# Kernel optimization log

Hardware: AMD Instinct MI355X
Metric: run time of the kernel (lower is better)

Reference implementation:

```python
import jax, jax.numpy as jnp
import numpy as np

B, N, D, H, DFF = 4096, 64, 256, 8, 1024
HD = D // H

def _ln(x, g, b):
    m = jnp.mean(x, axis=-1, keepdims=True)
    v = jnp.var(x, axis=-1, keepdims=True)
    return (x - m) / jnp.sqrt(v + 1e-5) * g + b


def setup_inputs() -> dict:
    key = jax.random.key(0)
    ks = jax.random.split(key, 16)
    s = jnp.float32(0.02)
    def rn(k, shape):
        return jax.random.normal(k, shape, dtype=jnp.float32) * s
    d2 = D // 2
    return {
        "x": jax.random.normal(ks[0], (B, N, 1), dtype=jnp.float32),
        "ve_w1": rn(ks[1], (1, d2)), "ve_b1": jnp.zeros((d2,), jnp.float32),
        "ve_w2": rn(ks[2], (d2, D)), "ve_b2": jnp.zeros((D,), jnp.float32),
        "pos_emb": rn(ks[3], (100, D)),
        "attn_in_w": rn(ks[4], (D, 3 * D)), "attn_in_b": jnp.zeros((3 * D,), jnp.float32),
        "attn_out_w": rn(ks[5], (D, D)), "attn_out_b": jnp.zeros((D,), jnp.float32),
        "ffn_w1": rn(ks[6], (D, DFF)), "ffn_b1": jnp.zeros((DFF,), jnp.float32),
        "ffn_w2": rn(ks[7], (DFF, D)), "ffn_b2": jnp.zeros((D,), jnp.float32),
        "ln1_g": jnp.ones((D,), jnp.float32), "ln1_b": jnp.zeros((D,), jnp.float32),
        "ln2_g": jnp.ones((D,), jnp.float32), "ln2_b": jnp.zeros((D,), jnp.float32),
        "rank_emb": rn(ks[8], (100, D)),
        "q_w": rn(ks[9], (D, D)), "q_b": jnp.zeros((D,), jnp.float32),
        "k_w": rn(ks[10], (D, D)), "k_b": jnp.zeros((D,), jnp.float32),
    }


def reference(x, ve_w1, ve_b1, ve_w2, ve_b2, pos_emb, attn_in_w, attn_in_b,
              attn_out_w, attn_out_b, ffn_w1, ffn_b1, ffn_w2, ffn_b2,
              ln1_g, ln1_b, ln2_g, ln2_b, rank_emb, q_w, q_b, k_w, k_b):
    # ---- encode ----
    v = jax.nn.relu(x @ ve_w1 + ve_b1) @ ve_w2 + ve_b2          # [B,N,D]
    h = v + pos_emb[:N][None]                                    # broadcast pos embed
    qkv = h @ attn_in_w + attn_in_b
    q, k, vv = jnp.split(qkv, 3, axis=-1)
    split_heads = lambda t: t.reshape(B, N, H, HD).transpose(0, 2, 1, 3)
    q, k, vv = split_heads(q), split_heads(k), split_heads(vv)
    scores = jnp.einsum('bhqd,bhkd->bhqk', q, k) / jnp.sqrt(jnp.float32(HD))
    attn = jax.nn.softmax(scores, axis=-1)
    ao = jnp.einsum('bhqk,bhkd->bhqd', attn, vv).transpose(0, 2, 1, 3).reshape(B, N, D)
    ao = ao @ attn_out_w + attn_out_b
    h = _ln(h + ao, ln1_g, ln1_b)
    ff = jax.nn.relu(h @ ffn_w1 + ffn_b1) @ ffn_w2 + ffn_b2
    enc = _ln(h + ff, ln2_g, ln2_b)                              # [B,N,D]

    # ---- pointer decode (greedy, coverage mask) ----
    Q = rank_emb[:N] @ q_w + q_b                                 # [N,D] rank queries
    K = enc @ k_w + k_b                                          # [B,N,D]
    base = jnp.einsum('td,bnd->tbn', Q, K)                       # [N,B,N] unmasked logits per rank
    bidx = jnp.arange(B)

    def step(mask, base_t):
        logits_t = jnp.where(mask > 0, base_t, -jnp.inf)         # masked_fill
        chosen = jnp.argmax(logits_t, axis=-1)                   # greedy pick
        mask = mask.at[bidx, chosen].set(0.0)                    # scatter mask update
        return mask, logits_t

    mask0 = jnp.ones((B, N), jnp.float32)
    _, all_logits = jax.lax.scan(step, mask0, base)              # [N,B,N]
    return all_logits.transpose(1, 0, 2)                         # [B,N,N]
```

## Files before the change

### kernel.cpp

```cpp
#include <hip/hip_runtime.h>
#include <math.h>


typedef __attribute__((ext_vector_type(8))) short bf16x8;
typedef __attribute__((ext_vector_type(4))) float f32x4;

#define NEG_FILL (-3.0e38f)

#define U_Q    0
#define U_VE   2048
#define U_QKV  6144
#define U_WO   30720
#define U_F1   38912
#define U_F2   71680
#define U_KW   104448
#define U_TOT  112640

#define SH_H  0
#define SH_A  16384
#define SH_SHORTS 32768
#define FB_FLOATS 4096
#define LDS_BYTES (SH_SHORTS*2 + FB_FLOATS*4)

__device__ __forceinline__ unsigned short f2bf(float f){
  unsigned u = __float_as_uint(f);
  return (unsigned short)((u + 0x7FFFu + ((u>>16)&1u)) >> 16);
}
__device__ __forceinline__ float bf2f(unsigned short h){
  return __uint_as_float(((unsigned)h) << 16);
}

#define MFMA(a,b,c) __builtin_amdgcn_mfma_f32_16x16x32_bf16((a),(b),(c),0,0,0)
#define SM_SCALE 0.17677669529663687f

__global__ void __launch_bounds__(256) prep_q(const float* __restrict__ rank_emb,
                                              const float* __restrict__ q_w,
                                              const float* __restrict__ q_b,
                                              short* __restrict__ wsp) {
    int t = blockIdx.x;
    int c = threadIdx.x;
    float acc = q_b[c];
    for (int d = 0; d < 256; d += 4) {
        acc += rank_emb[t*256 + d + 0] * q_w[(d+0)*256 + c]
             + rank_emb[t*256 + d + 1] * q_w[(d+1)*256 + c]
             + rank_emb[t*256 + d + 2] * q_w[(d+2)*256 + c]
             + rank_emb[t*256 + d + 3] * q_w[(d+3)*256 + c];
    }
    int kb = c >> 5, lane = ((c>>3)&3)*16 + (t&15), j = c & 7;
    int u = ((t>>4)*8 + kb)*64 + lane;
    wsp[(U_Q + u)*8 + j] = (short)f2bf(acc);
}

__global__ void __launch_bounds__(256) prep_w(const float* __restrict__ ve_w2,
                                              const float* __restrict__ attn_in_w,
                                              const float* __restrict__ attn_out_w,
                                              const float* __restrict__ ffn_w1,
                                              const float* __restrict__ ffn_w2,
                                              const float* __restrict__ k_w,
                                              short* __restrict__ wsp) {
    int r = blockIdx.x*256 + threadIdx.x;
    const float* w; int N, K, base;
    if (r < 4096)                { w = ve_w2;      N = 256;  K = 128;  base = U_VE;  }
    else if ((r -= 4096)  < 24576) { w = attn_in_w;  N = 768;  K = 256;  base = U_QKV; }
    else if ((r -= 24576) < 8192)  { w = attn_out_w; N = 256;  K = 256;  base = U_WO;  }
    else if ((r -= 8192)  < 32768) { w = ffn_w1;     N = 1024; K = 256;  base = U_F1;  }
    else if ((r -= 32768) < 32768) { w = ffn_w2;     N = 256;  K = 1024; base = U_F2;  }
    else     { r -= 32768;           w = k_w;        N = 256;  K = 256;  base = U_KW;  }
    int KB = K >> 5;
    int lane = r & 63;
    int kb   = (r >> 6) % KB;
    int nt   = r / (64 * KB);
    int n  = nt*16 + (lane & 15);
    int k0 = kb*32 + (lane >> 4)*8;
    bf16x8 hv;
#pragma unroll
    for (int j = 0; j < 8; j++) hv[j] = (short)f2bf(w[(size_t)(k0 + j)*N + n]);
    *(bf16x8*)&wsp[(size_t)(base + r) * 8] = hv;
}

__global__ void __launch_bounds__(512, 4) fused_kernel(
    const float* __restrict__ x,
    const float* __restrict__ ve_w1, const float* __restrict__ ve_b1,
    const float* __restrict__ ve_b2,
    const float* __restrict__ pos_emb,
    const float* __restrict__ attn_in_b,
    const float* __restrict__ attn_out_b,
    const float* __restrict__ ffn_b1, const float* __restrict__ ffn_b2,
    const float* __restrict__ ln1_g, const float* __restrict__ ln1_b,
    const float* __restrict__ ln2_g, const float* __restrict__ ln2_b,
    const float* __restrict__ k_b,
    const short* __restrict__ wsp,
    float* __restrict__ out)
{
    extern __shared__ short sm[];
    float* smf  = (float*)(sm + SH_SHORTS);
    float* SB   = smf;

    const int tid  = threadIdx.x;
    const int b    = blockIdx.x;
    const int w    = tid >> 6;
    const int lane = tid & 63;
    const int quad = lane >> 4;
    const int lcol = lane & 15;

    const bf16x8* wsv = (const bf16x8*)wsp;
    const bf16x8* HFu = (const bf16x8*)&sm[SH_H];
    bf16x8* HFw = (bf16x8*)&sm[SH_H];

#pragma unroll
    for (int i = 0; i < 2; i++) {
        int u = tid + i*512;
        int l3 = u & 63, kb = (u >> 6) & 3, mt = u >> 8;
        int m  = mt*16 + (l3 & 15);
        int k0 = kb*32 + (l3 >> 4)*8;
        float xv = x[b*64 + m];
        bf16x8 hv;
#pragma unroll
        for (int j = 0; j < 8; j++) {
            float f = xv * ve_w1[k0 + j] + ve_b1[k0 + j];
            hv[j] = (short)f2bf(f > 0.f ? f : 0.f);
        }
        *(bf16x8*)&sm[SH_A + u*8] = hv;
    }
    __syncthreads();

    {
        f32x4 acc[2][4];
#pragma unroll
        for (int s = 0; s < 2; s++)
#pragma unroll
            for (int mi = 0; mi < 4; mi++) acc[s][mi] = (f32x4){0.f,0.f,0.f,0.f};
#pragma unroll
        for (int kb = 0; kb < 4; kb++) {
            bf16x8 bh0 = wsv[U_VE + ((w    )*4+kb)*64 + lane];
            bf16x8 bh1 = wsv[U_VE + ((w + 8)*4+kb)*64 + lane];
#pragma unroll
            for (int mi = 0; mi < 4; mi++) {
                bf16x8 ah = *(const bf16x8*)&sm[SH_A + ((mi*4+kb)*64 + lane)*8];
                acc[0][mi] = MFMA(ah, bh0, acc[0][mi]);
                acc[1][mi] = MFMA(ah, bh1, acc[1][mi]);
            }
        }
        __syncthreads();
#pragma unroll
        for (int s = 0; s < 2; s++) {
            int n = (w + s*8)*16 + lcol;
#pragma unroll
            for (int mi = 0; mi < 4; mi++)
#pragma unroll
                for (int reg = 0; reg < 4; reg++) {
                    int m = mi*16 + quad*4 + reg;
                    float val = acc[s][mi][reg] + ve_b2[n] + pos_emb[m*256 + n];
                    int kb2 = n >> 5, l2 = ((n>>3)&3)*16 + (m&15), j2 = n & 7;
                    sm[SH_H + ((mi*8 + kb2)*64 + l2)*8 + j2] = (short)f2bf(val);
                }
        }
    }
    __syncthreads();

    f32x4 aoacc[2][4];
#pragma unroll
    for (int s = 0; s < 2; s++)
#pragma unroll
        for (int mi = 0; mi < 4; mi++) aoacc[s][mi] = (f32x4){0.f,0.f,0.f,0.f};

    const int il = w & 3;
    const int eo = il >> 1, ch = il & 1;

    auto qkv_phase = [&](int p) {
        int ntv = 32 + 4*p + il;
        if (w < 4) {
            int ntg = 4*p + il;
            f32x4 acc[4];
#pragma unroll
            for (int mi = 0; mi < 4; mi++) acc[mi] = (f32x4){0.f,0.f,0.f,0.f};
#pragma unroll
            for (int kb = 0; kb < 8; kb++) {
                bf16x8 bh = wsv[U_QKV + (ntg*8+kb)*64 + lane];
#pragma unroll
                for (int mi = 0; mi < 4; mi++)
                    acc[mi] = MFMA(HFu[(mi*8+kb)*64 + lane], bh, acc[mi]);
            }
#pragma unroll
            for (int mi = 0; mi < 4; mi++)
#pragma unroll
                for (int reg = 0; reg < 4; reg++) {
                    int m  = mi*16 + quad*4 + reg;
                    int cc = ch*16 + lcol;
                    short hv = (short)f2bf(acc[mi][reg] + attn_in_b[ntg*16 + lcol]);
                    int l2 = ((cc>>3)&3)*16 + (m&15), j2 = cc & 7;
                    sm[SH_A + eo*2048 + (mi*64 + l2)*8 + j2] = hv;
                }
            f32x4 va[2];
            va[0] = (f32x4){0.f,0.f,0.f,0.f}; va[1] = (f32x4){0.f,0.f,0.f,0.f};
#pragma unroll
            for (int kb = 0; kb < 8; kb++) {
                bf16x8 bh = wsv[U_QKV + (ntv*8+kb)*64 + lane];
                va[0] = MFMA(HFu[(0*8+kb)*64 + lane], bh, va[0]);
                va[1] = MFMA(HFu[(1*8+kb)*64 + lane], bh, va[1]);
            }
#pragma unroll
            for (int mi = 0; mi < 2; mi++)
#pragma unroll
                for (int reg = 0; reg < 4; reg++) {
                    int m  = mi*16 + quad*4 + reg;
                    int cc = ch*16 + lcol;
                    short hv = (short)f2bf(va[mi][reg] + attn_in_b[ntv*16 + lcol]);
                    int kb2 = m >> 5;
                    int l2 = ((m>>3)&3)*16 + lcol, j2 = m & 7;
                    sm[SH_A + 8192 + eo*2048 + ((ch*2 + kb2)*64 + l2)*8 + j2] = hv;
                }
        } else {
            int ntg = 16 + 4*p + il;
            f32x4 acc[4];
#pragma unroll
            for (int mi = 0; mi < 4; mi++) acc[mi] = (f32x4){0.f,0.f,0.f,0.f};
#pragma unroll
            for (int kb = 0; kb < 8; kb++) {
                bf16x8 bh = wsv[U_QKV + (ntg*8+kb)*64 + lane];
#pragma unroll
                for (int mi = 0; mi < 4; mi++)
                    acc[mi] = MFMA(HFu[(mi*8+kb)*64 + lane], bh, acc[mi]);
            }
#pragma unroll
            for (int mi = 0; mi < 4; mi++)
#pragma unroll
                for (int reg = 0; reg < 4; reg++) {
                    int m  = mi*16 + quad*4 + reg;
                    int cc = ch*16 + lcol;
                    short hv = (short)f2bf(acc[mi][reg] + attn_in_b[ntg*16 + lcol]);
                    int l2 = ((cc>>3)&3)*16 + (m&15), j2 = cc & 7;
                    sm[SH_A + 4096 + eo*2048 + ((m>>4)*64 + l2)*8 + j2] = hv;
                }
            f32x4 va[2];
            va[0] = (f32x4){0.f,0.f,0.f,0.f}; va[1] = (f32x4){0.f,0.f,0.f,0.f};
#pragma unroll
            for (int kb = 0; kb < 8; kb++) {
                bf16x8 bh = wsv[U_QKV + (ntv*8+kb)*64 + lane];
                va[0] = MFMA(HFu[(2*8+kb)*64 + lane], bh, va[0]);
                va[1] = MFMA(HFu[(3*8+kb)*64 + lane], bh, va[1]);
            }
#pragma unroll
            for (int mi2 = 0; mi2 < 2; mi2++)
#pragma unroll
                for (int reg = 0; reg < 4; reg++) {
                    int m  = (mi2+2)*16 + quad*4 + reg;
                    int cc = ch*16 + lcol;
                    short hv = (short)f2bf(va[mi2][reg] + attn_in_b[ntv*16 + lcol]);
                    int kb2 = m >> 5;
                    int l2 = ((m>>3)&3)*16 + lcol, j2 = m & 7;
                    sm[SH_A + 8192 + eo*2048 + ((ch*2 + kb2)*64 + l2)*8 + j2] = hv;
                }
        }
    };

    auto scores_sm = [&](int e) {
        if (w < 4) {
            int mi = w;
            bf16x8 ah = *(const bf16x8*)&sm[SH_A + e*2048 + (mi*64 + lane)*8];
            f32x4 sa[4];
#pragma unroll
            for (int ni = 0; ni < 4; ni++) {
                bf16x8 bh = *(const bf16x8*)&sm[SH_A + 4096 + e*2048 + (ni*64 + lane)*8];
                f32x4 z = (f32x4){0.f,0.f,0.f,0.f};
                sa[ni] = MFMA(ah, bh, z);
            }
#pragma unroll
            for (int reg = 0; reg < 4; reg++) {
                float v0 = sa[0][reg]*SM_SCALE, v1 = sa[1][reg]*SM_SCALE;
                float v2 = sa[2][reg]*SM_SCALE, v3 = sa[3][reg]*SM_SCALE;
                float mx = fmaxf(fmaxf(v0,v1), fmaxf(v2,v3));
#pragma unroll
                for (int off = 8; off >= 1; off >>= 1) mx = fmaxf(mx, __shfl_xor(mx, off, 64));
                v0 = __expf(v0-mx); v1 = __expf(v1-mx); v2 = __expf(v2-mx); v3 = __expf(v3-mx);
                float s = v0+v1+v2+v3;
#pragma unroll
                for (int off = 8; off >= 1; off >>= 1) s += __shfl_xor(s, off, 64);
                float inv = 1.0f / s;
                float pr[4] = {v0*inv, v1*inv, v2*inv, v3*inv};
                int mr = quad*4 + reg;
#pragma unroll
                for (int ni = 0; ni < 4; ni++) {
                    int u  = mi*2 + (ni>>1);
                    int l2 = ((ni*2 + (lcol>>3))&3)*16 + mr;
                    sm[SH_SHORTS + e*4096 + u*512 + l2*8 + (lcol&7)] = (short)f2bf(pr[ni]);
                }
            }
        }
    };

    auto pv_phase = [&](int e) {
        int mi = w & 3, ni = w >> 2;
        f32x4 pv = (f32x4){0.f,0.f,0.f,0.f};
#pragma unroll
        for (int kb = 0; kb < 2; kb++) {
            bf16x8 ah = *(const bf16x8*)&sm[SH_SHORTS + e*4096 + ((mi*2+kb)*64 + lane)*8];
            bf16x8 bh = *(const bf16x8*)&sm[SH_A + 8192 + e*2048 + ((ni*2+kb)*64 + lane)*8];
            pv = MFMA(ah, bh, pv);
        }
#pragma unroll
        for (int reg = 0; reg < 4; reg++) {
            int m = mi*16 + quad*4 + reg;
            int c = ni*16 + lcol;
            int l2 = ((c>>3)&3)*16 + (m&15), j2 = c & 7;
            sm[SH_A + 12288 + e*2048 + (mi*64 + l2)*8 + j2] = (short)f2bf(pv[reg]);
        }
    };

    auto wo_phase = [&](int hh, int e) {
        bf16x8 bh0 = wsv[U_WO + ((w    )*8 + hh)*64 + lane];
        bf16x8 bh1 = wsv[U_WO + ((w + 8)*8 + hh)*64 + lane];
#pragma unroll
        for (int mi = 0; mi < 4; mi++) {
            bf16x8 ah = *(const bf16x8*)&sm[SH_A + 12288 + e*2048 + (mi*64 + lane)*8];
            aoacc[0][mi] = MFMA(ah, bh0, aoacc[0][mi]);
            aoacc[1][mi] = MFMA(ah, bh1, aoacc[1][mi]);
        }
    };

    qkv_phase(0);
    __syncthreads();
    for (int p = 0; p < 4; p++) {
        scores_sm(0);
        __syncthreads();
        pv_phase(0);  scores_sm(1);
        __syncthreads();
        wo_phase(2*p, 0);  pv_phase(1);
        __syncthreads();
        wo_phase(2*p+1, 1);
        if (p < 3) qkv_phase(p+1);
        __syncthreads();
    }

#pragma unroll
    for (int s = 0; s < 2; s++) {
        int n = (w + s*8)*16 + lcol;
#pragma unroll
        for (int mi = 0; mi < 4; mi++)
#pragma unroll
            for (int reg = 0; reg < 4; reg++) {
                int m  = mi*16 + quad*4 + reg;
                int kb2 = n >> 5, l2 = ((n>>3)&3)*16 + (m&15), j2 = n & 7;
                int uu = ((mi*8 + kb2)*64 + l2)*8 + j2;
                float val = bf2f((unsigned short)sm[SH_H + uu]) + aoacc[s][mi][reg] + attn_out_b[n];
                sm[SH_H + uu] = (short)f2bf(val);
            }
    }
    __syncthreads();

    auto layernormFO = [&](const float* __restrict__ g, const float* __restrict__ bt) {
        int m = tid >> 3, kb = tid & 7;
        int ub = ((m>>4)*8 + kb)*64 + (m&15);
        bf16x8 h0 = HFu[ub +  0];
        bf16x8 h1 = HFu[ub + 16];
        bf16x8 h2 = HFu[ub + 32];
        bf16x8 h3 = HFu[ub + 48];
        float v[32];
#pragma unroll
        for (int j = 0; j < 8; j++) {
            v[j]    = bf2f((unsigned short)h0[j]);
            v[8+j]  = bf2f((unsigned short)h1[j]);
            v[16+j] = bf2f((unsigned short)h2[j]);
            v[24+j] = bf2f((unsigned short)h3[j]);
        }
        float sum = 0.f;
#pragma unroll
        for (int i = 0; i < 32; i++) sum += v[i];
#pragma unroll
        for (int off = 4; off >= 1; off >>= 1) sum += __shfl_xor(sum, off, 64);
        float mean = sum * (1.0f/256.0f);
        float s2 = 0.f;
#pragma unroll
        for (int i = 0; i < 32; i++) { float d = v[i] - mean; s2 += d*d; }
#pragma unroll
        for (int off = 4; off >= 1; off >>= 1) s2 += __shfl_xor(s2, off, 64);
        float r = 1.0f / sqrtf(s2 * (1.0f/256.0f) + 1e-5f);
#pragma unroll
        for (int q = 0; q < 4; q++) {
            bf16x8 oh;
#pragma unroll
            for (int j = 0; j < 8; j++) {
                int k = kb*32 + q*8 + j;
                oh[j] = (short)f2bf((v[q*8+j] - mean) * r * g[k] + bt[k]);
            }
            HFw[ub + q*16] = oh;
        }
        __syncthreads();
    };
    layernormFO(ln1_g, ln1_b);

    f32x4 f2acc[2][4];
#pragma unroll
    for (int s = 0; s < 2; s++)
#pragma unroll
        for (int mi = 0; mi < 4; mi++) f2acc[s][mi] = (f32x4){0.f,0.f,0.f,0.f};

    for (int c = 0; c < 4; c++) {
        f32x4 a1[4];
#pragma unroll
        for (int mi = 0; mi < 4; mi++) a1[mi] = (f32x4){0.f,0.f,0.f,0.f};
#pragma unroll
        for (int kb = 0; kb < 8; kb++) {
            bf16x8 bh = wsv[U_F1 + ((c*16 + w)*8 + kb)*64 + lane];
#pragma unroll
            for (int mi = 0; mi < 4; mi++) {
                bf16x8 ah = HFu[(mi*8+kb)*64 + lane];
                a1[mi] = MFMA(ah, bh, a1[mi]);
            }
        }
        __syncthreads();
#pragma unroll
        for (int mi = 0; mi < 4; mi++)
#pragma unroll
            for (int reg = 0; reg < 4; reg++) {
                int m = mi*16 + quad*4 + reg;
                int n = (c*16 + w)*16 + lcol;
                float val = a1[mi][reg] + ffn_b1[n];
                val = val > 0.f ? val : 0.f;
                int kk = w*16 + lcol;
                int kb2 = kk >> 5, l2 = ((kk>>3)&3)*16 + (m&15), j2 = kk & 7;
                sm[SH_A + ((mi*8 + kb2)*64 + l2)*8 + j2] = (short)f2bf(val);
            }
#pragma unroll
        for (int mi = 0; mi < 4; mi++) a1[mi] = (f32x4){0.f,0.f,0.f,0.f};
#pragma unroll
        for (int kb = 0; kb < 8; kb++) {
            bf16x8 bh = wsv[U_F1 + ((c*16 + w + 8)*8 + kb)*64 + lane];
#pragma unroll
            for (int mi = 0; mi < 4; mi++) {
                bf16x8 ah = HFu[(mi*8+kb)*64 + lane];
                a1[mi] = MFMA(ah, bh, a1[mi]);
            }
        }
#pragma unroll
        for (int mi = 0; mi < 4; mi++)
#pragma unroll
            for (int reg = 0; reg < 4; reg++) {
                int m = mi*16 + quad*4 + reg;
                int n = (c*16 + w + 8)*16 + lcol;
                float val = a1[mi][reg] + ffn_b1[n];
                val = val > 0.f ? val : 0.f;
                int kk = (w + 8)*16 + lcol;
                int kb2 = kk >> 5, l2 = ((kk>>3)&3)*16 + (m&15), j2 = kk & 7;
                sm[SH_A + ((mi*8 + kb2)*64 + l2)*8 + j2] = (short)f2bf(val);
            }
        __syncthreads();
#pragma unroll 2
        for (int kbl = 0; kbl < 8; kbl++) {
            bf16x8 bh0 = wsv[U_F2 + ((w    )*32 + c*8 + kbl)*64 + lane];
            bf16x8 bh1 = wsv[U_F2 + ((w + 8)*32 + c*8 + kbl)*64 + lane];
#pragma unroll
            for (int mi = 0; mi < 4; mi++) {
                bf16x8 ah = *(const bf16x8*)&sm[SH_A + ((mi*8+kbl)*64 + lane)*8];
                f2acc[0][mi] = MFMA(ah, bh0, f2acc[0][mi]);
                f2acc[1][mi] = MFMA(ah, bh1, f2acc[1][mi]);
            }
        }
    }
    __syncthreads();
#pragma unroll
    for (int s = 0; s < 2; s++) {
        int n = (w + s*8)*16 + lcol;
#pragma unroll
        for (int mi = 0; mi < 4; mi++)
#pragma unroll
            for (int reg = 0; reg < 4; reg++) {
                int m  = mi*16 + quad*4 + reg;
                int kb2 = n >> 5, l2 = ((n>>3)&3)*16 + (m&15), j2 = n & 7;
                int uu = ((mi*8 + kb2)*64 + l2)*8 + j2;
                float val = bf2f((unsigned short)sm[SH_H + uu]) + f2acc[s][mi][reg] + ffn_b2[n];
                sm[SH_H + uu] = (short)f2bf(val);
            }
    }
    __syncthreads();
    layernormFO(ln2_g, ln2_b);

    {
        f32x4 kacc[2][4];
#pragma unroll
        for (int s = 0; s < 2; s++)
#pragma unroll
            for (int mi = 0; mi < 4; mi++) kacc[s][mi] = (f32x4){0.f,0.f,0.f,0.f};
#pragma unroll
        for (int kb = 0; kb < 8; kb++) {
            bf16x8 bh0 = wsv[U_KW + ((w    )*8+kb)*64 + lane];
            bf16x8 bh1 = wsv[U_KW + ((w + 8)*8+kb)*64 + lane];
#pragma unroll
            for (int mi = 0; mi < 4; mi++) {
                bf16x8 ah = HFu[(mi*8+kb)*64 + lane];
                kacc[0][mi] = MFMA(ah, bh0, kacc[0][mi]);
                kacc[1][mi] = MFMA(ah, bh1, kacc[1][mi]);
            }
        }
        __syncthreads();
#pragma unroll
        for (int s = 0; s < 2; s++) {
            int n = (w + s*8)*16 + lcol;
#pragma unroll
            for (int mi = 0; mi < 4; mi++)
#pragma unroll
                for (int reg = 0; reg < 4; reg++) {
                    int m = mi*16 + quad*4 + reg;
                    int nt2 = m >> 4, kb2 = n >> 5;
                    int l2 = ((n>>3)&3)*16 + (m&15), j2 = n & 7;
                    sm[SH_H + ((nt2*8 + kb2)*64 + l2)*8 + j2] =
                        (short)f2bf(kacc[s][mi][reg] + k_b[n]);
                }
        }
    }
    __syncthreads();

#pragma unroll
    for (int it = 0; it < 2; it++) {
        int t = w*2 + it;
        int mi = t >> 2, nt = t & 3;
        f32x4 sacc = (f32x4){0.f,0.f,0.f,0.f};
#pragma unroll
        for (int kb = 0; kb < 8; kb++) {
            bf16x8 bh = HFu[(nt*8+kb)*64 + lane];
            bf16x8 ah = wsv[U_Q + (mi*8+kb)*64 + lane];
            sacc = MFMA(ah, bh, sacc);
        }
#pragma unroll
        for (int reg = 0; reg < 4; reg++) {
            int tt = mi*16 + quad*4 + reg;
            int n = nt*16 + lcol;
            SB[tt*64 + (n ^ ((tt&7)<<2))] = sacc[reg];
        }
    }
    __syncthreads();

    if (tid < 64) {
        int ln = tid;
        bool alive = true;
        float* outb = out + (size_t)b * (64*64);
        for (int t = 0; t < 64; t++) {
            float v  = SB[t*64 + (ln ^ ((t&7)<<2))];
            float lv = alive ? v : NEG_FILL;
            outb[t*64 + ln] = lv;
            float bv = lv;
#pragma unroll
            for (int off = 32; off >= 1; off >>= 1)
                bv = fmaxf(bv, __shfl_xor(bv, off, 64));
            unsigned long long mk = __ballot(lv == bv);
            int bi = __ffsll(mk) - 1;
            if (bi == ln) alive = false;
        }
    }
}

extern "C" void kernel_launch(void* const* d_in, const int* in_sizes, int n_in,
                              void* d_out, int out_size, void* d_ws, size_t ws_size,
                              hipStream_t stream) {
    (void)in_sizes; (void)n_in; (void)out_size; (void)ws_size;
    const float* x          = (const float*)d_in[0];
    const float* ve_w1      = (const float*)d_in[1];
    const float* ve_b1      = (const float*)d_in[2];
    const float* ve_w2      = (const float*)d_in[3];
    const float* ve_b2      = (const float*)d_in[4];
    const float* pos_emb    = (const float*)d_in[5];
    const float* attn_in_w  = (const float*)d_in[6];
    const float* attn_in_b  = (const float*)d_in[7];
    const float* attn_out_w = (const float*)d_in[8];
    const float* attn_out_b = (const float*)d_in[9];
    const float* ffn_w1     = (const float*)d_in[10];
    const float* ffn_b1     = (const float*)d_in[11];
    const float* ffn_w2     = (const float*)d_in[12];
    const float* ffn_b2     = (const float*)d_in[13];
    const float* ln1_g      = (const float*)d_in[14];
    const float* ln1_b      = (const float*)d_in[15];
    const float* ln2_g      = (const float*)d_in[16];
    const float* ln2_b      = (const float*)d_in[17];
    const float* rank_emb   = (const float*)d_in[18];
    const float* q_w        = (const float*)d_in[19];
    const float* q_b        = (const float*)d_in[20];
    const float* k_w        = (const float*)d_in[21];
    const float* k_b        = (const float*)d_in[22];
    float* outp = (float*)d_out;
    short* wsp  = (short*)d_ws;

    (void)hipFuncSetAttribute((const void*)fused_kernel,
                              hipFuncAttributeMaxDynamicSharedMemorySize,
                              (int)LDS_BYTES);

    hipLaunchKernelGGL(prep_q, dim3(64), dim3(256), 0, stream, rank_emb, q_w, q_b, wsp);
    hipLaunchKernelGGL(prep_w, dim3(432), dim3(256), 0, stream,
                       ve_w2, attn_in_w, attn_out_w, ffn_w1, ffn_w2, k_w, wsp);
    hipLaunchKernelGGL(fused_kernel, dim3(4096), dim3(512), LDS_BYTES, stream,
                       x, ve_w1, ve_b1, ve_b2, pos_emb,
                       attn_in_b, attn_out_b,
                       ffn_b1, ffn_b2,
                       ln1_g, ln1_b, ln2_g, ln2_b,
                       k_b, (const short*)wsp, outp);
}
```

Baseline: 934.2 us.

## XOR-swizzle LDS fragment layout and pack bf16 pairs on conversion

Applies an XOR swizzle (lane ^ (lane>>4)) to every shared-memory bf16 fragment buffer, on both the scatter writes and the MFMA operand reads, so the strided scalar stores from accumulator tiles spread across LDS banks instead of colliding. The float-to-bf16 conversions are reorganized to convert pairs at once and hoist bias loads out of inner loops, and the V-transpose stores become 32-bit writes. The swizzle must match exactly across every producer and consumer of each buffer, which adds index arithmetic and risks correctness if any path is missed.

```diff
diff --git a/kernel.cpp b/kernel.cpp
--- a/kernel.cpp
+++ b/kernel.cpp
@@ -4,6 +4,7 @@
 
 typedef __attribute__((ext_vector_type(8))) short bf16x8;
 typedef __attribute__((ext_vector_type(4))) float f32x4;
+typedef __attribute__((ext_vector_type(4))) unsigned u32x4;
 
 #define NEG_FILL (-3.0e38f)
 
@@ -28,6 +29,9 @@
 }
 __device__ __forceinline__ float bf2f(unsigned short h){
   return __uint_as_float(((unsigned)h) << 16);
+}
+__device__ __forceinline__ unsigned pk2(float a, float b){
+  return (unsigned)f2bf(a) | ((unsigned)f2bf(b) << 16);
 }
 
 #define MFMA(a,b,c) __builtin_amdgcn_mfma_f32_16x16x32_bf16((a),(b),(c),0,0,0)
@@ -102,10 +106,10 @@
     const int lane = tid & 63;
     const int quad = lane >> 4;
     const int lcol = lane & 15;
+    const int slane = lane ^ (lane >> 4);
 
     const bf16x8* wsv = (const bf16x8*)wsp;
     const bf16x8* HFu = (const bf16x8*)&sm[SH_H];
-    bf16x8* HFw = (bf16x8*)&sm[SH_H];
 
 #pragma unroll
     for (int i = 0; i < 2; i++) {
@@ -114,13 +118,17 @@
         int m  = mt*16 + (l3 & 15);
         int k0 = kb*32 + (l3 >> 4)*8;
         float xv = x[b*64 + m];
-        bf16x8 hv;
+        float f[8];
 #pragma unroll
         for (int j = 0; j < 8; j++) {
-            float f = xv * ve_w1[k0 + j] + ve_b1[k0 + j];
-            hv[j] = (short)f2bf(f > 0.f ? f : 0.f);
-        }
-        *(bf16x8*)&sm[SH_A + u*8] = hv;
+            float t0 = xv * ve_w1[k0 + j] + ve_b1[k0 + j];
+            f[j] = t0 > 0.f ? t0 : 0.f;
+        }
+        u32x4 hv;
+        hv[0] = pk2(f[0], f[1]); hv[1] = pk2(f[2], f[3]);
+        hv[2] = pk2(f[4], f[5]); hv[3] = pk2(f[6], f[7]);
+        int sl3 = l3 ^ (l3 >> 4);
+        *(u32x4*)&sm[SH_A + ((u & ~63) | sl3)*8] = hv;
     }
     __syncthreads();
 
@@ -136,7 +144,7 @@
             bf16x8 bh1 = wsv[U_VE + ((w + 8)*4+kb)*64 + lane];
 #pragma unroll
             for (int mi = 0; mi < 4; mi++) {
-                bf16x8 ah = *(const bf16x8*)&sm[SH_A + ((mi*4+kb)*64 + lane)*8];
+                bf16x8 ah = *(const bf16x8*)&sm[SH_A + ((mi*4+kb)*64 + slane)*8];
                 acc[0][mi] = MFMA(ah, bh0, acc[0][mi]);
                 acc[1][mi] = MFMA(ah, bh1, acc[1][mi]);
             }
@@ -145,15 +153,24 @@
 #pragma unroll
         for (int s = 0; s < 2; s++) {
             int n = (w + s*8)*16 + lcol;
-#pragma unroll
-            for (int mi = 0; mi < 4; mi++)
+            int hi = (n>>3)&3, kb2 = n>>5, j2 = n&7;
+#pragma unroll
+            for (int mi = 0; mi < 4; mi++) {
+                float vv[4];
 #pragma unroll
                 for (int reg = 0; reg < 4; reg++) {
                     int m = mi*16 + quad*4 + reg;
-                    float val = acc[s][mi][reg] + ve_b2[n] + pos_emb[m*256 + n];
-                    int kb2 = n >> 5, l2 = ((n>>3)&3)*16 + (m&15), j2 = n & 7;
-                    sm[SH_H + ((mi*8 + kb2)*64 + l2)*8 + j2] = (short)f2bf(val);
-                }
+                    vv[reg] = acc[s][mi][reg] + ve_b2[n] + pos_emb[m*256 + n];
+                }
+#pragma unroll
+                for (int rp = 0; rp < 2; rp++) {
+                    unsigned r = pk2(vv[2*rp], vv[2*rp+1]);
+                    int m0 = quad*4 + 2*rp;
+                    int gbase = (mi*8 + kb2)*64 + hi*16;
+                    sm[SH_H + (gbase + ((m0  )^hi))*8 + j2] = (short)r;
+                    sm[SH_H + (gbase + ((m0+1)^hi))*8 + j2] = (short)(r >> 16);
+                }
+            }
         }
     }
     __syncthreads();
@@ -169,6 +186,8 @@
 
     auto qkv_phase = [&](int p) {
         int ntv = 32 + 4*p + il;
+        int cc = ch*16 + lcol;
+        int hic = (cc>>3)&3, j2c = cc&7;
         if (w < 4) {
             int ntg = 4*p + il;
             f32x4 acc[4];
@@ -179,36 +198,38 @@
                 bf16x8 bh = wsv[U_QKV + (ntg*8+kb)*64 + lane];
 #pragma unroll
                 for (int mi = 0; mi < 4; mi++)
-                    acc[mi] = MFMA(HFu[(mi*8+kb)*64 + lane], bh, acc[mi]);
-            }
+                    acc[mi] = MFMA(HFu[(mi*8+kb)*64 + slane], bh, acc[mi]);
+            }
+            float bq = attn_in_b[ntg*16 + lcol];
 #pragma unroll
             for (int mi = 0; mi < 4; mi++)
 #pragma unroll
-                for (int reg = 0; reg < 4; reg++) {
-                    int m  = mi*16 + quad*4 + reg;
-                    int cc = ch*16 + lcol;
-                    short hv = (short)f2bf(acc[mi][reg] + attn_in_b[ntg*16 + lcol]);
-                    int l2 = ((cc>>3)&3)*16 + (m&15), j2 = cc & 7;
-                    sm[SH_A + eo*2048 + (mi*64 + l2)*8 + j2] = hv;
+                for (int rp = 0; rp < 2; rp++) {
+                    unsigned r = pk2(acc[mi][2*rp] + bq, acc[mi][2*rp+1] + bq);
+                    int m0 = quad*4 + 2*rp;
+                    int gbase = SH_A + eo*2048 + (mi*64 + hic*16)*8;
+                    sm[gbase + (((m0  )^hic))*8 + j2c] = (short)r;
+                    sm[gbase + (((m0+1)^hic))*8 + j2c] = (short)(r >> 16);
                 }
             f32x4 va[2];
             va[0] = (f32x4){0.f,0.f,0.f,0.f}; va[1] = (f32x4){0.f,0.f,0.f,0.f};
 #pragma unroll
             for (int kb = 0; kb < 8; kb++) {
                 bf16x8 bh = wsv[U_QKV + (ntv*8+kb)*64 + lane];
-                va[0] = MFMA(HFu[(0*8+kb)*64 + lane], bh, va[0]);
-                va[1] = MFMA(HFu[(1*8+kb)*64 + lane], bh, va[1]);
-            }
+                va[0] = MFMA(HFu[(0*8+kb)*64 + slane], bh, va[0]);
+                va[1] = MFMA(HFu[(1*8+kb)*64 + slane], bh, va[1]);
+            }
+            float bv = attn_in_b[ntv*16 + lcol];
 #pragma unroll
             for (int mi = 0; mi < 2; mi++)
 #pragma unroll
-                for (int reg = 0; reg < 4; reg++) {
-                    int m  = mi*16 + quad*4 + reg;
-                    int cc = ch*16 + lcol;
-                    short hv = (short)f2bf(va[mi][reg] + attn_in_b[ntv*16 + lcol]);
-                    int kb2 = m >> 5;
-                    int l2 = ((m>>3)&3)*16 + lcol, j2 = m & 7;
-                    sm[SH_A + 8192 + eo*2048 + ((ch*2 + kb2)*64 + l2)*8 + j2] = hv;
+                for (int rp = 0; rp < 2; rp++) {
+                    unsigned r = pk2(va[mi][2*rp] + bv, va[mi][2*rp+1] + bv);
+                    int m0 = mi*16 + quad*4 + 2*rp;
+                    int kb2 = m0>>5, hi2 = (m0>>3)&3;
+                    int X = SH_A + 8192 + eo*2048
+                          + (((ch*2 + kb2)*64 + hi2*16 + (lcol^hi2)))*8 + (m0&7);
+                    *(unsigned*)&sm[X] = r;
                 }
         } else {
             int ntg = 16 + 4*p + il;
@@ -220,36 +241,38 @@
                 bf16x8 bh = wsv[U_QKV + (ntg*8+kb)*64 + lane];
 #pragma unroll
                 for (int mi = 0; mi < 4; mi++)
-                    acc[mi] = MFMA(HFu[(mi*8+kb)*64 + lane], bh, acc[mi]);
-            }
+                    acc[mi] = MFMA(HFu[(mi*8+kb)*64 + slane], bh, acc[mi]);
+            }
+            float bk = attn_in_b[ntg*16 + lcol];
 #pragma unroll
             for (int mi = 0; mi < 4; mi++)
 #pragma unroll
-                for (int reg = 0; reg < 4; reg++) {
-                    int m  = mi*16 + quad*4 + reg;
-                    int cc = ch*16 + lcol;
-                    short hv = (short)f2bf(acc[mi][reg] + attn_in_b[ntg*16 + lcol]);
-                    int l2 = ((cc>>3)&3)*16 + (m&15), j2 = cc & 7;
-                    sm[SH_A + 4096 + eo*2048 + ((m>>4)*64 + l2)*8 + j2] = hv;
+                for (int rp = 0; rp < 2; rp++) {
+                    unsigned r = pk2(acc[mi][2*rp] + bk, acc[mi][2*rp+1] + bk);
+                    int m0 = quad*4 + 2*rp;
+                    int gbase = SH_A + 4096 + eo*2048 + (mi*64 + hic*16)*8;
+                    sm[gbase + (((m0  )^hic))*8 + j2c] = (short)r;
+                    sm[gbase + (((m0+1)^hic))*8 + j2c] = (short)(r >> 16);
                 }
             f32x4 va[2];
             va[0] = (f32x4){0.f,0.f,0.f,0.f}; va[1] = (f32x4){0.f,0.f,0.f,0.f};
 #pragma unroll
             for (int kb = 0; kb < 8; kb++) {
                 bf16x8 bh = wsv[U_QKV + (ntv*8+kb)*64 + lane];
-                va[0] = MFMA(HFu[(2*8+kb)*64 + lane], bh, va[0]);
-                va[1] = MFMA(HFu[(3*8+kb)*64 + lane], bh, va[1]);
-            }
+                va[0] = MFMA(HFu[(2*8+kb)*64 + slane], bh, va[0]);
+                va[1] = MFMA(HFu[(3*8+kb)*64 + slane], bh, va[1]);
+            }
+            float bv = attn_in_b[ntv*16 + lcol];
 #pragma unroll
             for (int mi2 = 0; mi2 < 2; mi2++)
 #pragma unroll
-                for (int reg = 0; reg < 4; reg++) {
-                    int m  = (mi2+2)*16 + quad*4 + reg;
-                    int cc = ch*16 + lcol;
-                    short hv = (short)f2bf(va[mi2][reg] + attn_in_b[ntv*16 + lcol]);
-                    int kb2 = m >> 5;
-                    int l2 = ((m>>3)&3)*16 + lcol, j2 = m & 7;
-                    sm[SH_A + 8192 + eo*2048 + ((ch*2 + kb2)*64 + l2)*8 + j2] = hv;
+                for (int rp = 0; rp < 2; rp++) {
+                    unsigned r = pk2(va[mi2][2*rp] + bv, va[mi2][2*rp+1] + bv);
+                    int m0 = (mi2+2)*16 + quad*4 + 2*rp;
+                    int kb2 = m0>>5, hi2 = (m0>>3)&3;
+                    int X = SH_A + 8192 + eo*2048
+                          + (((ch*2 + kb2)*64 + hi2*16 + (lcol^hi2)))*8 + (m0&7);
+                    *(unsigned*)&sm[X] = r;
                 }
         }
     };
@@ -257,14 +280,17 @@
     auto scores_sm = [&](int e) {
         if (w < 4) {
             int mi = w;
-            bf16x8 ah = *(const bf16x8*)&sm[SH_A + e*2048 + (mi*64 + lane)*8];
+            bf16x8 ah = *(const bf16x8*)&sm[SH_A + e*2048 + (mi*64 + slane)*8];
             f32x4 sa[4];
 #pragma unroll
             for (int ni = 0; ni < 4; ni++) {
-                bf16x8 bh = *(const bf16x8*)&sm[SH_A + 4096 + e*2048 + (ni*64 + lane)*8];
+                bf16x8 bh = *(const bf16x8*)&sm[SH_A + 4096 + e*2048 + (ni*64 + slane)*8];
                 f32x4 z = (f32x4){0.f,0.f,0.f,0.f};
                 sa[ni] = MFMA(ah, bh, z);
             }
+            int lo3 = lcol>>3, j2 = lcol&7;
+            int hiA = lo3, hiB = 2 + lo3;
+            int pbase = SH_SHORTS + e*4096;
 #pragma unroll
             for (int reg = 0; reg < 4; reg++) {
                 float v0 = sa[0][reg]*SM_SCALE, v1 = sa[1][reg]*SM_SCALE;
@@ -277,14 +303,13 @@
 #pragma unroll
                 for (int off = 8; off >= 1; off >>= 1) s += __shfl_xor(s, off, 64);
                 float inv = 1.0f / s;
-                float pr[4] = {v0*inv, v1*inv, v2*inv, v3*inv};
                 int mr = quad*4 + reg;
-#pragma unroll
-                for (int ni = 0; ni < 4; ni++) {
-                    int u  = mi*2 + (ni>>1);
-                    int l2 = ((ni*2 + (lcol>>3))&3)*16 + mr;
-                    sm[SH_SHORTS + e*4096 + u*512 + l2*8 + (lcol&7)] = (short)f2bf(pr[ni]);
-                }
+                unsigned r01 = pk2(v0*inv, v1*inv);
+                unsigned r23 = pk2(v2*inv, v3*inv);
+                sm[pbase + ((mi*2+0)*64 + hiA*16 + (mr^hiA))*8 + j2] = (short)r01;
+                sm[pbase + ((mi*2+0)*64 + hiB*16 + (mr^hiB))*8 + j2] = (short)(r01 >> 16);
+                sm[pbase + ((mi*2+1)*64 + hiA*16 + (mr^hiA))*8 + j2] = (short)r23;
+                sm[pbase + ((mi*2+1)*64 + hiB*16 + (mr^hiB))*8 + j2] = (short)(r23 >> 16);
             }
         }
     };
@@ -294,16 +319,18 @@
         f32x4 pv = (f32x4){0.f,0.f,0.f,0.f};
 #pragma unroll
         for (int kb = 0; kb < 2; kb++) {
-            bf16x8 ah = *(const bf16x8*)&sm[SH_SHORTS + e*4096 + ((mi*2+kb)*64 + lane)*8];
-            bf16x8 bh = *(const bf16x8*)&sm[SH_A + 8192 + e*2048 + ((ni*2+kb)*64 + lane)*8];
+            bf16x8 ah = *(const bf16x8*)&sm[SH_SHORTS + e*4096 + ((mi*2+kb)*64 + slane)*8];
+            bf16x8 bh = *(const bf16x8*)&sm[SH_A + 8192 + e*2048 + ((ni*2+kb)*64 + slane)*8];
             pv = MFMA(ah, bh, pv);
         }
-#pragma unroll
-        for (int reg = 0; reg < 4; reg++) {
-            int m = mi*16 + quad*4 + reg;
-            int c = ni*16 + lcol;
-            int l2 = ((c>>3)&3)*16 + (m&15), j2 = c & 7;
-            sm[SH_A + 12288 + e*2048 + (mi*64 + l2)*8 + j2] = (short)f2bf(pv[reg]);
+        int hi = (ni*2 + (lcol>>3))&3, j2 = lcol&7;
+#pragma unroll
+        for (int rp = 0; rp < 2; rp++) {
+            unsigned r = pk2(pv[2*rp], pv[2*rp+1]);
+            int m0 = quad*4 + 2*rp;
+            int gbase = SH_A + 12288 + e*2048 + (mi*64 + hi*16)*8;
+            sm[gbase + (((m0  )^hi))*8 + j2] = (short)r;
+            sm[gbase + (((m0+1)^hi))*8 + j2] = (short)(r >> 16);
         }
     };
 
@@ -312,7 +339,7 @@
         bf16x8 bh1 = wsv[U_WO + ((w + 8)*8 + hh)*64 + lane];
 #pragma unroll
         for (int mi = 0; mi < 4; mi++) {
-            bf16x8 ah = *(const bf16x8*)&sm[SH_A + 12288 + e*2048 + (mi*64 + lane)*8];
+            bf16x8 ah = *(const bf16x8*)&sm[SH_A + 12288 + e*2048 + (mi*64 + slane)*8];
             aoacc[0][mi] = MFMA(ah, bh0, aoacc[0][mi]);
             aoacc[1][mi] = MFMA(ah, bh1, aoacc[1][mi]);
         }
@@ -335,26 +362,37 @@
 #pragma unroll
     for (int s = 0; s < 2; s++) {
         int n = (w + s*8)*16 + lcol;
-#pragma unroll
-        for (int mi = 0; mi < 4; mi++)
+        int hi = (n>>3)&3, kb2 = n>>5, j2 = n&7;
+        float bo = attn_out_b[n];
+#pragma unroll
+        for (int mi = 0; mi < 4; mi++) {
+            float vv[4];
 #pragma unroll
             for (int reg = 0; reg < 4; reg++) {
-                int m  = mi*16 + quad*4 + reg;
-                int kb2 = n >> 5, l2 = ((n>>3)&3)*16 + (m&15), j2 = n & 7;
-                int uu = ((mi*8 + kb2)*64 + l2)*8 + j2;
-                float val = bf2f((unsigned short)sm[SH_H + uu]) + aoacc[s][mi][reg] + attn_out_b[n];
-                sm[SH_H + uu] = (short)f2bf(val);
-            }
+                int m0 = quad*4 + reg;
+                int idx = SH_H + ((mi*8 + kb2)*64 + hi*16 + (m0^hi))*8 + j2;
+                vv[reg] = bf2f((unsigned short)sm[idx]) + aoacc[s][mi][reg] + bo;
+            }
+#pragma unroll
+            for (int rp = 0; rp < 2; rp++) {
+                unsigned r = pk2(vv[2*rp], vv[2*rp+1]);
+                int m0 = quad*4 + 2*rp;
+                int gbase = (mi*8 + kb2)*64 + hi*16;
+                sm[SH_H + (gbase + ((m0  )^hi))*8 + j2] = (short)r;
+                sm[SH_H + (gbase + ((m0+1)^hi))*8 + j2] = (short)(r >> 16);
+            }
+        }
     }
     __syncthreads();
 
     auto layernormFO = [&](const float* __restrict__ g, const float* __restrict__ bt) {
         int m = tid >> 3, kb = tid & 7;
-        int ub = ((m>>4)*8 + kb)*64 + (m&15);
-        bf16x8 h0 = HFu[ub +  0];
-        bf16x8 h1 = HFu[ub + 16];
-        bf16x8 h2 = HFu[ub + 32];
-        bf16x8 h3 = HFu[ub + 48];
+        int gb = ((m>>4)*8 + kb)*64;
+        int low = m & 15;
+        bf16x8 h0 = HFu[gb + 0*16 + (low^0)];
+        bf16x8 h1 = HFu[gb + 1*16 + (low^1)];
+        bf16x8 h2 = HFu[gb + 2*16 + (low^2)];
+        bf16x8 h3 = HFu[gb + 3*16 + (low^3)];
         float v[32];
 #pragma unroll
         for (int j = 0; j < 8; j++) {
@@ -377,13 +415,16 @@
         float r = 1.0f / sqrtf(s2 * (1.0f/256.0f) + 1e-5f);
 #pragma unroll
         for (int q = 0; q < 4; q++) {
-            bf16x8 oh;
+            float o[8];
 #pragma unroll
             for (int j = 0; j < 8; j++) {
                 int k = kb*32 + q*8 + j;
-                oh[j] = (short)f2bf((v[q*8+j] - mean) * r * g[k] + bt[k]);
-            }
-            HFw[ub + q*16] = oh;
+                o[j] = (v[q*8+j] - mean) * r * g[k] + bt[k];
+            }
+            u32x4 po;
+            po[0] = pk2(o[0], o[1]); po[1] = pk2(o[2], o[3]);
+            po[2] = pk2(o[4], o[5]); po[3] = pk2(o[6], o[7]);
+            *(u32x4*)&sm[SH_H + (gb + q*16 + (low^q))*8] = po;
         }
         __syncthreads();
     };
@@ -404,23 +445,29 @@
             bf16x8 bh = wsv[U_F1 + ((c*16 + w)*8 + kb)*64 + lane];
 #pragma unroll
             for (int mi = 0; mi < 4; mi++) {
-                bf16x8 ah = HFu[(mi*8+kb)*64 + lane];
+                bf16x8 ah = HFu[(mi*8+kb)*64 + slane];
                 a1[mi] = MFMA(ah, bh, a1[mi]);
             }
         }
         __syncthreads();
-#pragma unroll
-        for (int mi = 0; mi < 4; mi++)
-#pragma unroll
-            for (int reg = 0; reg < 4; reg++) {
-                int m = mi*16 + quad*4 + reg;
-                int n = (c*16 + w)*16 + lcol;
-                float val = a1[mi][reg] + ffn_b1[n];
-                val = val > 0.f ? val : 0.f;
-                int kk = w*16 + lcol;
-                int kb2 = kk >> 5, l2 = ((kk>>3)&3)*16 + (m&15), j2 = kk & 7;
-                sm[SH_A + ((mi*8 + kb2)*64 + l2)*8 + j2] = (short)f2bf(val);
-            }
+        {
+            int n = (c*16 + w)*16 + lcol;
+            int kk = w*16 + lcol;
+            int hi = (kk>>3)&3, kb2 = kk>>5, j2 = kk&7;
+            float bf1 = ffn_b1[n];
+#pragma unroll
+            for (int mi = 0; mi < 4; mi++)
+#pragma unroll
+                for (int rp = 0; rp < 2; rp++) {
+                    float x0 = a1[mi][2*rp]   + bf1; x0 = x0 > 0.f ? x0 : 0.f;
+                    float x1 = a1[mi][2*rp+1] + bf1; x1 = x1 > 0.f ? x1 : 0.f;
+                    unsigned r = pk2(x0, x1);
+                    int m0 = quad*4 + 2*rp;
+                    int gbase = (mi*8 + kb2)*64 + hi*16;
+                    sm[SH_A + (gbase + ((m0  )^hi))*8 + j2] = (short)r;
+                    sm[SH_A + (gbase + ((m0+1)^hi))*8 + j2] = (short)(r >> 16);
+                }
+        }
 #pragma unroll
         for (int mi = 0; mi < 4; mi++) a1[mi] = (f32x4){0.f,0.f,0.f,0.f};
 #pragma unroll
@@ -428,22 +475,28 @@
             bf16x8 bh = wsv[U_F1 + ((c*16 + w + 8)*8 + kb)*64 + lane];
 #pragma unroll
             for (int mi = 0; mi < 4; mi++) {
-                bf16x8 ah = HFu[(mi*8+kb)*64 + lane];
+                bf16x8 ah = HFu[(mi*8+kb)*64 + slane];
                 a1[mi] = MFMA(ah, bh, a1[mi]);
             }
         }
-#pragma unroll
-        for (int mi = 0; mi < 4; mi++)
-#pragma unroll
-            for (int reg = 0; reg < 4; reg++) {
-                int m = mi*16 + quad*4 + reg;
-                int n = (c*16 + w + 8)*16 + lcol;
-                float val = a1[mi][reg] + ffn_b1[n];
-                val = val > 0.f ? val : 0.f;
-                int kk = (w + 8)*16 + lcol;
-                int kb2 = kk >> 5, l2 = ((kk>>3)&3)*16 + (m&15), j2 = kk & 7;
-                sm[SH_A + ((mi*8 + kb2)*64 + l2)*8 + j2] = (short)f2bf(val);
-            }
+        {
+            int n = (c*16 + w + 8)*16 + lcol;
+            int kk = (w + 8)*16 + lcol;
+            int hi = (kk>>3)&3, kb2 = kk>>5, j2 = kk&7;
+            float bf1 = ffn_b1[n];
+#pragma unroll
+            for (int mi = 0; mi < 4; mi++)
+#pragma unroll
+                for (int rp = 0; rp < 2; rp++) {
+                    float x0 = a1[mi][2*rp]   + bf1; x0 = x0 > 0.f ? x0 : 0.f;
+                    float x1 = a1[mi][2*rp+1] + bf1; x1 = x1 > 0.f ? x1 : 0.f;
+                    unsigned r = pk2(x0, x1);
+                    int m0 = quad*4 + 2*rp;
+                    int gbase = (mi*8 + kb2)*64 + hi*16;
+                    sm[SH_A + (gbase + ((m0  )^hi))*8 + j2] = (short)r;
+                    sm[SH_A + (gbase + ((m0+1)^hi))*8 + j2] = (short)(r >> 16);
+                }
+        }
         __syncthreads();
 #pragma unroll 2
         for (int kbl = 0; kbl < 8; kbl++) {
@@ -451,7 +504,7 @@
             bf16x8 bh1 = wsv[U_F2 + ((w + 8)*32 + c*8 + kbl)*64 + lane];
 #pragma unroll
             for (int mi = 0; mi < 4; mi++) {
-                bf16x8 ah = *(const bf16x8*)&sm[SH_A + ((mi*8+kbl)*64 + lane)*8];
+                bf16x8 ah = *(const bf16x8*)&sm[SH_A + ((mi*8+kbl)*64 + slane)*8];
                 f2acc[0][mi] = MFMA(ah, bh0, f2acc[0][mi]);
                 f2acc[1][mi] = MFMA(ah, bh1, f2acc[1][mi]);
             }
@@ -461,16 +514,26 @@
 #pragma unroll
     for (int s = 0; s < 2; s++) {
         int n = (w + s*8)*16 + lcol;
-#pragma unroll
-        for (int mi = 0; mi < 4; mi++)
+        int hi = (n>>3)&3, kb2 = n>>5, j2 = n&7;
+        float bo = ffn_b2[n];
+#pragma unroll
+        for (int mi = 0; mi < 4; mi++) {
+            float vv[4];
 #pragma unroll
             for (int reg = 0; reg < 4; reg++) {
-                int m  = mi*16 + quad*4 + reg;
-                int kb2 = n >> 5, l2 = ((n>>3)&3)*16 + (m&15), j2 = n & 7;
-                int uu = ((mi*8 + kb2)*64 + l2)*8 + j2;
-                float val = bf2f((unsigned short)sm[SH_H + uu]) + f2acc[s][mi][reg] + ffn_b2[n];
-                sm[SH_H + uu] = (short)f2bf(val);
-            }
+                int m0 = quad*4 + reg;
+                int idx = SH_H + ((mi*8 + kb2)*64 + hi*16 + (m0^hi))*8 + j2;
+                vv[reg] = bf2f((unsigned short)sm[idx]) + f2acc[s][mi][reg] + bo;
+            }
+#pragma unroll
+            for (int rp = 0; rp < 2; rp++) {
+                unsigned r = pk2(vv[2*rp], vv[2*rp+1]);
+                int m0 = quad*4 + 2*rp;
+                int gbase = (mi*8 + kb2)*64 + hi*16;
+                sm[SH_H + (gbase + ((m0  )^hi))*8 + j2] = (short)r;
+                sm[SH_H + (gbase + ((m0+1)^hi))*8 + j2] = (short)(r >> 16);
+            }
+        }
     }
     __syncthreads();
     layernormFO(ln2_g, ln2_b);
@@ -487,7 +550,7 @@
             bf16x8 bh1 = wsv[U_KW + ((w + 8)*8+kb)*64 + lane];
 #pragma unroll
             for (int mi = 0; mi < 4; mi++) {
-                bf16x8 ah = HFu[(mi*8+kb)*64 + lane];
+                bf16x8 ah = HFu[(mi*8+kb)*64 + slane];
                 kacc[0][mi] = MFMA(ah, bh0, kacc[0][mi]);
                 kacc[1][mi] = MFMA(ah, bh1, kacc[1][mi]);
             }
@@ -496,15 +559,17 @@
 #pragma unroll
         for (int s = 0; s < 2; s++) {
             int n = (w + s*8)*16 + lcol;
+            int hi = (n>>3)&3, kb2 = n>>5, j2 = n&7;
+            float bk = k_b[n];
 #pragma unroll
             for (int mi = 0; mi < 4; mi++)
 #pragma unroll
-                for (int reg = 0; reg < 4; reg++) {
-                    int m = mi*16 + quad*4 + reg;
-                    int nt2 = m >> 4, kb2 = n >> 5;
-                    int l2 = ((n>>3)&3)*16 + (m&15), j2 = n & 7;
-                    sm[SH_H + ((nt2*8 + kb2)*64 + l2)*8 + j2] =
-                        (short)f2bf(kacc[s][mi][reg] + k_b[n]);
+                for (int rp = 0; rp < 2; rp++) {
+                    unsigned r = pk2(kacc[s][mi][2*rp] + bk, kacc[s][mi][2*rp+1] + bk);
+                    int m0 = quad*4 + 2*rp;
+                    int gbase = (mi*8 + kb2)*64 + hi*16;
+                    sm[SH_H + (gbase + ((m0  )^hi))*8 + j2] = (short)r;
+                    sm[SH_H + (gbase + ((m0+1)^hi))*8 + j2] = (short)(r >> 16);
                 }
         }
     }
@@ -517,7 +582,7 @@
         f32x4 sacc = (f32x4){0.f,0.f,0.f,0.f};
 #pragma unroll
         for (int kb = 0; kb < 8; kb++) {
-            bf16x8 bh = HFu[(nt*8+kb)*64 + lane];
+            bf16x8 bh = HFu[(nt*8+kb)*64 + slane];
             bf16x8 ah = wsv[U_Q + (mi*8+kb)*64 + lane];
             sacc = MFMA(ah, bh, sacc);
         }
```

New measurement: 1.243 ms. 33.1% more time.
